# Performance work log

Hardware: AMD Instinct MI355X
Metric: run time of the kernel (lower is better)

## Reference

```python
import jax, jax.numpy as jnp
import numpy as np

# Module hyperparameters (from init_kwargs)
P_GEN = 0.2
P_MEM = 0.1
B, C, H, W = 128, 256, 32, 32
FIXED = int(P_GEN * C)  # generalization channels, always active
MEM = C - FIXED          # memorization channels, per-example Bernoulli(P_MEM)


def setup_inputs() -> dict:
    key = jax.random.key(0)
    k1, k2 = jax.random.split(key)
    X = jax.random.normal(k1, (B, C, H, W), dtype=jnp.float32)
    indices = jax.random.randint(k2, (B,), 0, 60000, dtype=jnp.int64)
    return {"X": X, "indices": indices}


def _example_mask(idx):
    # Deterministic per-example mask: Philox key folded with the sample index
    # replaces the torch CPU Generator(manual_seed=sample_idx).
    k = jax.random.fold_in(jax.random.key(42), idx)
    mem = jax.random.bernoulli(k, P_MEM, (MEM,)).astype(jnp.float32)
    return jnp.concatenate([jnp.ones((FIXED,), jnp.float32), mem])  # [C]


def reference(X, indices):
    # Training-mode path: per-example channel mask, broadcast over H, W.
    masks = jax.vmap(_example_mask)(indices)  # [B, C]
    return X * masks[:, :, None, None]
```

## Files before the change

### kernel.cpp

```cpp
#include <hip/hip_runtime.h>
#include <stdint.h>


#define BDIM   128
#define CDIM   256
#define HWDIM  1024
#define FIXEDC 51
#define MEMC   205

__device__ __forceinline__ uint32_t rotl32(uint32_t x, int d) {
    return (x << d) | (x >> (32 - d));
}

__device__ __forceinline__ void threefry2x32_block(uint32_t k0, uint32_t k1,
                                                   uint32_t c0, uint32_t c1,
                                                   uint32_t& o0, uint32_t& o1) {
    const uint32_t ks0 = k0, ks1 = k1, ks2 = k0 ^ k1 ^ 0x1BD11BDAu;
    uint32_t x0 = c0 + ks0;
    uint32_t x1 = c1 + ks1;
#define TF_R4(r0, r1, r2, r3)                              \
    x0 += x1; x1 = rotl32(x1, r0); x1 ^= x0;               \
    x0 += x1; x1 = rotl32(x1, r1); x1 ^= x0;               \
    x0 += x1; x1 = rotl32(x1, r2); x1 ^= x0;               \
    x0 += x1; x1 = rotl32(x1, r3); x1 ^= x0;
    TF_R4(13, 15, 26, 6);  x0 += ks1; x1 += ks2 + 1u;
    TF_R4(17, 29, 16, 24); x0 += ks2; x1 += ks0 + 2u;
    TF_R4(13, 15, 26, 6);  x0 += ks0; x1 += ks1 + 3u;
    TF_R4(17, 29, 16, 24); x0 += ks1; x1 += ks2 + 4u;
    TF_R4(13, 15, 26, 6);  x0 += ks2; x1 += ks0 + 5u;
#undef TF_R4
    o0 = x0;
    o1 = x1;
}

__device__ __forceinline__ float bits_to_mask(uint32_t bits) {
    uint32_t fb = (bits >> 9) | 0x3f800000u;
    float u = __uint_as_float(fb) - 1.0f;
    return (u < 0.1f) ? 1.0f : 0.0f;
}

__global__ void tied_dropout_mask_kernel(const int* __restrict__ indices,
                                         float* __restrict__ mask) {
    const int b = blockIdx.x;
    const int t = threadIdx.x;

    const uint32_t id = (uint32_t)indices[b];
    uint32_t fk0, fk1;
    threefry2x32_block(0u, 42u, 0u, id, fk0, fk1);

    float* mrow = mask + b * CDIM;
    if (t < FIXEDC) mrow[t] = 1.0f;

    if (t < MEMC) {
        uint32_t y0, y1;
        threefry2x32_block(fk0, fk1, 0u, (uint32_t)t, y0, y1);
        mrow[FIXEDC + t] = bits_to_mask(y0 ^ y1);
    }
}

__global__ void tied_dropout_mul_kernel(const float4* __restrict__ X,
                                        const float* __restrict__ mask,
                                        float4* __restrict__ out,
                                        int total4) {
    const int stride = gridDim.x * blockDim.x;
    for (int i = blockIdx.x * blockDim.x + threadIdx.x; i < total4; i += stride) {
        const int bc = i >> 8;
        const float m = mask[bc];
        float4 v = X[i];
        v.x *= m; v.y *= m; v.z *= m; v.w *= m;
        out[i] = v;
    }
}

extern "C" void kernel_launch(void* const* d_in, const int* in_sizes, int n_in,
                              void* d_out, int out_size, void* d_ws, size_t ws_size,
                              hipStream_t stream) {
    const float* X = (const float*)d_in[0];
    const int* indices = (const int*)d_in[1];
    float* out = (float*)d_out;
    float* mask = (float*)d_ws;

    tied_dropout_mask_kernel<<<BDIM, 256, 0, stream>>>(indices, mask);

    const int total4 = BDIM * CDIM * HWDIM / 4;
    tied_dropout_mul_kernel<<<2048, 256, 0, stream>>>(
        (const float4*)X, mask, (float4*)out, total4);
}
```

Measured before the change: 51.56 us.

## Fuse mask generation into multiply kernel with per-block channel groups

Merges the separate mask-generation and multiply kernels into one launch. Each block covers four channel planes of one example, computes their Threefry mask values in registers and scales four float4 per thread, writing with nontemporal stores. This removes a kernel launch, the workspace mask round trip and per-element mask loads. The cost is redundant key derivation and hashing in every block, and a much larger grid of small blocks.

```diff
diff --git a/kernel.cpp b/kernel.cpp
--- a/kernel.cpp
+++ b/kernel.cpp
@@ -4,9 +4,12 @@
 
 #define BDIM   128
 #define CDIM   256
-#define HWDIM  1024
 #define FIXEDC 51
-#define MEMC   205
+#define CPB    4
+#define GROUPS (CDIM / CPB)
+#define F4_PER_PLANE 256
+
+typedef float floatx4 __attribute__((ext_vector_type(4)));
 
 __device__ __forceinline__ uint32_t rotl32(uint32_t x, int d) {
     return (x << d) | (x >> (32 - d));
@@ -39,50 +42,49 @@
     return (u < 0.1f) ? 1.0f : 0.0f;
 }
 
-__global__ void tied_dropout_mask_kernel(const int* __restrict__ indices,
-                                         float* __restrict__ mask) {
-    const int b = blockIdx.x;
+__global__ __launch_bounds__(256) void tied_dropout_fused_kernel(
+        const floatx4* __restrict__ X,
+        const int* __restrict__ indices,
+        floatx4* __restrict__ out) {
+    const int g = blockIdx.x;
+    const int b = g >> 6;
+    const int c0 = (g & 63) * CPB;
     const int t = threadIdx.x;
 
     const uint32_t id = (uint32_t)indices[b];
     uint32_t fk0, fk1;
     threefry2x32_block(0u, 42u, 0u, id, fk0, fk1);
 
-    float* mrow = mask + b * CDIM;
-    if (t < FIXEDC) mrow[t] = 1.0f;
+    float m[CPB];
+#pragma unroll
+    for (int j = 0; j < CPB; ++j) {
+        const int c = c0 + j;
+        if (c < FIXEDC) {
+            m[j] = 1.0f;
+        } else {
+            uint32_t y0, y1;
+            threefry2x32_block(fk0, fk1, 0u, (uint32_t)(c - FIXEDC), y0, y1);
+            m[j] = bits_to_mask(y0 ^ y1);
+        }
+    }
 
-    if (t < MEMC) {
-        uint32_t y0, y1;
-        threefry2x32_block(fk0, fk1, 0u, (uint32_t)t, y0, y1);
-        mrow[FIXEDC + t] = bits_to_mask(y0 ^ y1);
-    }
-}
-
-__global__ void tied_dropout_mul_kernel(const float4* __restrict__ X,
-                                        const float* __restrict__ mask,
-                                        float4* __restrict__ out,
-                                        int total4) {
-    const int stride = gridDim.x * blockDim.x;
-    for (int i = blockIdx.x * blockDim.x + threadIdx.x; i < total4; i += stride) {
-        const int bc = i >> 8;
-        const float m = mask[bc];
-        float4 v = X[i];
-        v.x *= m; v.y *= m; v.z *= m; v.w *= m;
-        out[i] = v;
+    const int base = g * (CPB * F4_PER_PLANE) + t;
+#pragma unroll
+    for (int j = 0; j < CPB; ++j) {
+        const int i = base + j * F4_PER_PLANE;
+        floatx4 v = X[i];
+        v *= m[j];
+        __builtin_nontemporal_store(v, &out[i]);
     }
 }
 
 extern "C" void kernel_launch(void* const* d_in, const int* in_sizes, int n_in,
                               void* d_out, int out_size, void* d_ws, size_t ws_size,
                               hipStream_t stream) {
-    const float* X = (const float*)d_in[0];
+    const floatx4* X = (const floatx4*)d_in[0];
     const int* indices = (const int*)d_in[1];
-    float* out = (float*)d_out;
-    float* mask = (float*)d_ws;
+    floatx4* out = (floatx4*)d_out;
 
-    tied_dropout_mask_kernel<<<BDIM, 256, 0, stream>>>(indices, mask);
-
-    const int total4 = BDIM * CDIM * HWDIM / 4;
-    tied_dropout_mul_kernel<<<2048, 256, 0, stream>>>(
-        (const float4*)X, mask, (float4*)out, total4);
+    const int nblocks = BDIM * GROUPS;
+    tied_dropout_fused_kernel<<<nblocks, 256, 0, stream>>>(X, indices, out);
 }
```

New measurement: 44.52 us. 1.16x faster.
